# Kernel optimization log

Hardware: AMD Instinct MI355X
Metric: run time of the kernel (lower is better)

The kernel has to match this reference:

```python
import jax, jax.numpy as jnp
import numpy as np

B, S, D, H, HD = 4, 2048, 1024, 16, 64
MLP = 4 * D
ROPE_BASE = 10000.0
TARGET_SPARSITY = 0.2


def _rotate_half(t):
    return jnp.concatenate([-t[..., HD // 2:], t[..., :HD // 2]], axis=-1)


def setup_inputs() -> dict:
    key = jax.random.key(0)
    ks = jax.random.split(key, 10)
    s = 0.02
    return {
        "x": jax.random.normal(ks[0], (B, S, D), jnp.float32),
        "gate_w": jax.random.normal(ks[1], (D, 1), jnp.float32) * s,
        "gate_b": jnp.zeros((1,), jnp.float32),
        "wq": jax.random.normal(ks[2], (D, D), jnp.float32) * s,
        "wk": jax.random.normal(ks[3], (D, D), jnp.float32) * s,
        "wv": jax.random.normal(ks[4], (D, D), jnp.float32) * s,
        "wo": jax.random.normal(ks[5], (D, D), jnp.float32) * s,
        "conv_w": jax.random.normal(ks[6], (D, 3), jnp.float32) * s,  # depthwise k=3
        "conv_b": jnp.zeros((D,), jnp.float32),
        "mlp_w1": jax.random.normal(ks[7], (D, MLP), jnp.float32) * s,
        "mlp_b1": jnp.zeros((MLP,), jnp.float32),
        "mlp_w2": jax.random.normal(ks[8], (MLP, D), jnp.float32) * s,
        "mlp_b2": jnp.zeros((D,), jnp.float32),
    }


def reference(x, gate_w, gate_b, wq, wk, wv, wo, conv_w, conv_b,
              mlp_w1, mlp_b1, mlp_w2, mlp_b2):
    # --- Router (eval path: hard threshold, mask_ste == active mask) ---
    logits = x @ gate_w + gate_b                    # [B,S,1]
    probs = jax.nn.sigmoid(logits)
    aux_loss = (probs.mean() - TARGET_SPARSITY) ** 2
    mask = (probs > 0.5).astype(x.dtype)            # [B,S,1]

    # --- Reflexive stream: causal depthwise conv (left pad 2) + MLP ---
    xp = jnp.pad(x, ((0, 0), (2, 0), (0, 0)))       # [B,S+2,D]
    x_conv = (xp[:, 0:S] * conv_w[:, 0]
              + xp[:, 1:S + 1] * conv_w[:, 1]
              + xp[:, 2:S + 2] * conv_w[:, 2] + conv_b)
    shallow = jax.nn.relu(x_conv @ mlp_w1 + mlp_b1) @ mlp_w2 + mlp_b2

    # --- Contextual stream: RoPE causal attention, queries gated by router ---
    q = (x @ wq).reshape(B, S, H, HD)
    k = (x @ wk).reshape(B, S, H, HD)
    v = (x @ wv).reshape(B, S, H, HD)

    pos = jnp.arange(S)
    inv_freq = 1.0 / (ROPE_BASE ** (jnp.arange(0, HD, 2, dtype=jnp.float32) / HD))
    freqs = pos[:, None].astype(jnp.float32) * inv_freq[None, :]
    emb = jnp.concatenate([freqs, freqs], axis=-1)  # [S,HD]
    cos = jnp.cos(emb)[None, :, None, :]
    sin = jnp.sin(emb)[None, :, None, :]
    q = q * cos + _rotate_half(q) * sin
    k = k * cos + _rotate_half(k) * sin

    scale = 1.0 / np.sqrt(HD)
    scores = jnp.einsum('bqhd,bkhd->bhqk', q, k) * scale
    causal = pos[:, None] >= pos[None, :]           # [S,S]
    scores = jnp.where(causal[None, None], scores, jnp.finfo(scores.dtype).min)
    attn = jax.nn.softmax(scores, axis=-1)
    ctx = jnp.einsum('bhqk,bkhd->bqhd', attn, v).reshape(B, S, D)
    ctx = (ctx @ wo) * mask                         # scatter back: only active queries contribute

    out = x + shallow + ctx
    return out, aux_loss
```

## Files before the change

### kernel.cpp

```cpp
#include <hip/hip_runtime.h>
#include <hip/hip_bf16.h>

#define DDIM 1024
#define SLEN 2048
#define NTOK 8192
#define MLPD 4096

typedef float f32x4 __attribute__((ext_vector_type(4)));
typedef __bf16 bf16x8 __attribute__((ext_vector_type(8)));

__device__ __forceinline__ void async16(void* lds, const void* g) {
  __builtin_amdgcn_global_load_lds(
      (__attribute__((address_space(1))) void*)g,
      (__attribute__((address_space(3))) void*)lds, 16, 0, 0);
}

__global__ __launch_bounds__(256) void prep_kernel(
    const float* __restrict__ x, const float* __restrict__ gate_w,
    const float* __restrict__ gate_b, const float* __restrict__ conv_w,
    const float* __restrict__ conv_b, __bf16* __restrict__ xb,
    __bf16* __restrict__ xcb, float* __restrict__ maskp,
    float* __restrict__ probsp) {
  const int tok = blockIdx.x, t = threadIdx.x;
  const int s = tok & (SLEN - 1);
  const float* xr = x + (size_t)tok * DDIM;
  float4 v = ((const float4*)xr)[t];
  float4 g = ((const float4*)gate_w)[t];
  float part = v.x * g.x + v.y * g.y + v.z * g.z + v.w * g.w;
#pragma unroll
  for (int d = 32; d; d >>= 1) part += __shfl_down(part, d);
  __shared__ float ws4[4];
  const int lane = t & 63, w = t >> 6;
  if (lane == 0) ws4[w] = part;
  __syncthreads();
  if (t == 0) {
    float logit = ws4[0] + ws4[1] + ws4[2] + ws4[3] + gate_b[0];
    float prob = 1.f / (1.f + __expf(-logit));
    probsp[tok] = prob;
    maskp[tok] = prob > 0.5f ? 1.f : 0.f;
  }
  union { ushort4 u; __bf16 b[4]; } xo;
  xo.b[0] = (__bf16)v.x; xo.b[1] = (__bf16)v.y;
  xo.b[2] = (__bf16)v.z; xo.b[3] = (__bf16)v.w;
  ((ushort4*)(xb + (size_t)tok * DDIM))[t] = xo.u;
  float4 zero4 = {0.f, 0.f, 0.f, 0.f};
  float4 m1 = (s >= 1) ? ((const float4*)(xr - DDIM))[t] : zero4;
  float4 m2 = (s >= 2) ? ((const float4*)(xr - 2 * DDIM))[t] : zero4;
  int d0 = t * 4;
  float vv[4] = {v.x, v.y, v.z, v.w};
  float a1[4] = {m1.x, m1.y, m1.z, m1.w};
  float a2[4] = {m2.x, m2.y, m2.z, m2.w};
  union { ushort4 u; __bf16 b[4]; } co;
#pragma unroll
  for (int i = 0; i < 4; ++i) {
    float c0 = conv_w[(d0 + i) * 3 + 0];
    float c1 = conv_w[(d0 + i) * 3 + 1];
    float c2 = conv_w[(d0 + i) * 3 + 2];
    float r = a2[i] * c0 + a1[i] * c1 + vv[i] * c2 + conv_b[d0 + i];
    co.b[i] = (__bf16)r;
  }
  ((ushort4*)(xcb + (size_t)tok * DDIM))[t] = co.u;
}

__global__ __launch_bounds__(256) void tcast_kernel(const float* __restrict__ src,
                                                    __bf16* __restrict__ dst,
                                                    int K, int N) {
  __shared__ __bf16 tile[64][65];
  const int n0 = blockIdx.x * 64, k0 = blockIdx.y * 64;
  const int t = threadIdx.x;
  const int cr = (t & 15) * 4;
#pragma unroll
  for (int i = 0; i < 4; ++i) {
    int rr = (t >> 4) + i * 16;
    float4 v = *(const float4*)(src + (size_t)(k0 + rr) * N + n0 + cr);
    tile[rr][cr + 0] = (__bf16)v.x; tile[rr][cr + 1] = (__bf16)v.y;
    tile[rr][cr + 2] = (__bf16)v.z; tile[rr][cr + 3] = (__bf16)v.w;
  }
  __syncthreads();
#pragma unroll
  for (int i = 0; i < 2; ++i) {
    int c = t + i * 256;
    int nl = c >> 3, koff = (c & 7) * 8;
    union { uint4 u; __bf16 b[8]; } o;
#pragma unroll
    for (int j = 0; j < 8; ++j) o.b[j] = tile[koff + j][nl];
    *(uint4*)(dst + (size_t)(n0 + nl) * K + k0 + koff) = o.u;
  }
}

template <int EPI>
__global__ __launch_bounds__(256, 3) void gemm_bt(
    const __bf16* __restrict__ A, const __bf16* __restrict__ Bt,
    const float* __restrict__ bias, const float* __restrict__ xres,
    const float* __restrict__ maskp, __bf16* __restrict__ Cb,
    float* __restrict__ Cf, int M, int N, int K) {
  __shared__ char smem[32768];
  char* As = smem;
  char* Bs = smem + 16384;
  const int t = threadIdx.x, lane = t & 63, w = t >> 6;
  const int m0 = blockIdx.y * 128, n0 = blockIdx.x * 128;
  const int wm = (w >> 1) * 64, wn = (w & 1) * 64;
  f32x4 acc[4][4] = {};
  const int nk = K >> 6;
  for (int kt = 0; kt < nk; ++kt) {
    const int k0 = kt << 6;
#pragma unroll
    for (int rd = 0; rd < 4; ++rd) {
      int o = ((rd * 4 + w) << 10) + (lane << 4);
      int row = o >> 7;
      int us = ((o >> 4) & 7) ^ (row & 7);
      async16(As + o, A + (size_t)(m0 + row) * K + k0 + us * 8);
      async16(Bs + o, Bt + (size_t)(n0 + row) * K + k0 + us * 8);
    }
    __syncthreads();
#pragma unroll
    for (int ks = 0; ks < 2; ++ks) {
      bf16x8 af[4], bfr[4];
#pragma unroll
      for (int mt = 0; mt < 4; ++mt) {
        int row = wm + mt * 16 + (lane & 15);
        int u = (ks * 4 + (lane >> 4)) ^ (row & 7);
        af[mt] = *(const bf16x8*)(As + row * 128 + u * 16);
      }
#pragma unroll
      for (int nt = 0; nt < 4; ++nt) {
        int row = wn + nt * 16 + (lane & 15);
        int u = (ks * 4 + (lane >> 4)) ^ (row & 7);
        bfr[nt] = *(const bf16x8*)(Bs + row * 128 + u * 16);
      }
#pragma unroll
      for (int mt = 0; mt < 4; ++mt)
#pragma unroll
        for (int nt = 0; nt < 4; ++nt)
          acc[mt][nt] = __builtin_amdgcn_mfma_f32_16x16x32_bf16(
              af[mt], bfr[nt], acc[mt][nt], 0, 0, 0);
    }
    __syncthreads();
  }
#pragma unroll
  for (int mt = 0; mt < 4; ++mt)
#pragma unroll
    for (int nt = 0; nt < 4; ++nt)
#pragma unroll
      for (int r = 0; r < 4; ++r) {
        int row = m0 + wm + mt * 16 + ((lane >> 4) << 2) + r;
        int col = n0 + wn + nt * 16 + (lane & 15);
        float v = acc[mt][nt][r];
        size_t idx = (size_t)row * N + col;
        if constexpr (EPI == 0) {
          Cb[idx] = (__bf16)v;
        } else if constexpr (EPI == 1) {
          v += bias[col];
          Cb[idx] = (__bf16)fmaxf(v, 0.f);
        } else if constexpr (EPI == 2) {
          Cf[idx] = xres[idx] + v + bias[col];
        } else {
          Cf[idx] += maskp[row] * v;
        }
      }
}

__global__ __launch_bounds__(256) void rope_kernel(__bf16* __restrict__ qkv) {
  const int tok = blockIdx.x, t = threadIdx.x;
  const int s = tok & (SLEN - 1);
#pragma unroll
  for (int pp = 0; pp < 2; ++pp) {
    int p = t + pp * 256;
    int h = p >> 5, i = p & 31;
    float invf = __powf(10000.f, -(float)i * (1.f / 32.f));
    float fr = (float)s * invf;
    float sn = sinf(fr), cs = cosf(fr);
    __bf16* qp = qkv + (size_t)tok * 3072 + h * 64 + i;
    float xq = (float)qp[0], yq = (float)qp[32];
    qp[0] = (__bf16)(xq * cs - yq * sn);
    qp[32] = (__bf16)(yq * cs + xq * sn);
    __bf16* kp = qp + 1024;
    float xk = (float)kp[0], yk = (float)kp[32];
    kp[0] = (__bf16)(xk * cs - yk * sn);
    kp[32] = (__bf16)(yk * cs + xk * sn);
  }
}

__device__ __forceinline__ void scatterV(char* Vdst, int w, int lane,
                                         float4 va, float4 vb) {
  union { float4 f; __bf16 bv[8]; } u0, u1;
  u0.f = va; u1.f = vb;
#pragma unroll
  for (int j = 0; j < 8; ++j) {
    int d = w * 8 + j;
    int by = d * 128 + (((lane >> 3) ^ (d & 7)) << 4) + ((lane & 7) << 1);
    *(__bf16*)(Vdst + by) = u0.bv[j];
    int d2 = d + 32;
    int by2 = d2 * 128 + (((lane >> 3) ^ (d2 & 7)) << 4) + ((lane & 7) << 1);
    *(__bf16*)(Vdst + by2) = u1.bv[j];
  }
}

__global__ __launch_bounds__(256, 3) void attn_kernel(const __bf16* __restrict__ qkv,
                                                      __bf16* __restrict__ ctx) {
  __shared__ char sm[49152];
  const int t = threadIdx.x, lane = t & 63, w = t >> 6;
  const int c = lane & 15, g = lane >> 4, g4 = g * 4;
  const int bh = blockIdx.y, h = bh & 15, b = bh >> 4;
  const size_t tokbase = (size_t)b * SLEN;
  const __bf16* qg = qkv + tokbase * 3072 + h * 64;
  const __bf16* kg = qg + 1024;
  const __bf16* vg = qg + 2048;
  const float SCL = 0.125f * 1.44269504f;
  char* Ps = sm + (w << 12);

  for (int ph = 0; ph < 2; ++ph) {
    const int qt = ph == 0 ? (int)blockIdx.x : 15 - (int)blockIdx.x;
    const int q0 = qt * 128;
    int cur = 0;
#pragma unroll
    for (int rd = 0; rd < 4; ++rd) {
      int o = ((rd * 4 + w) << 10) + (lane << 4);
      int row = o >> 7;
      int us = ((o >> 4) & 7) ^ (row & 7);
      async16(sm + o, qg + (size_t)(q0 + row) * 3072 + us * 8);
    }
#pragma unroll
    for (int rd = 0; rd < 2; ++rd) {
      int o = ((rd * 4 + w) << 10) + (lane << 4);
      int row = o >> 7;
      int us = ((o >> 4) & 7) ^ (row & 7);
      async16(sm + 16384 + o, kg + (size_t)row * 3072 + us * 8);
    }
    {
      float4 va = *(const float4*)(vg + (size_t)lane * 3072 + w * 8);
      float4 vb2 = *(const float4*)(vg + (size_t)lane * 3072 + w * 8 + 32);
      scatterV(sm + 32768, w, lane, va, vb2);
    }
    __syncthreads();
    bf16x8 qb[2][2];
#pragma unroll
    for (int mt = 0; mt < 2; ++mt)
#pragma unroll
      for (int ks = 0; ks < 2; ++ks) {
        int row = w * 32 + mt * 16 + c;
        int u = (ks * 4 + g) ^ (row & 7);
        qb[mt][ks] = *(const bf16x8*)(sm + row * 128 + u * 16);
      }

    float m_run[2] = {-1e30f, -1e30f}, l_run[2] = {0.f, 0.f};
    f32x4 o_acc[2][4] = {};
    const int nkt = (q0 + 128) >> 6;
    const int wrow0 = q0 + w * 32;

    for (int kt = 0; kt < nkt; ++kt) {
      const int k0 = kt << 6;
      char* Kc = sm + 16384 + cur * 8192;
      char* Vc = sm + 32768 + cur * 8192;
      const bool pref = (kt + 1) < nkt;
      float4 va, vb2;
      if (pref) {
        const int kn0 = k0 + 64;
        char* Kn = sm + 16384 + (cur ^ 1) * 8192;
#pragma unroll
        for (int rd = 0; rd < 2; ++rd) {
          int o = ((rd * 4 + w) << 10) + (lane << 4);
          int row = o >> 7;
          int us = ((o >> 4) & 7) ^ (row & 7);
          async16(Kn + o, kg + (size_t)(kn0 + row) * 3072 + us * 8);
        }
        va = *(const float4*)(vg + (size_t)(kn0 + lane) * 3072 + w * 8);
        vb2 = *(const float4*)(vg + (size_t)(kn0 + lane) * 3072 + w * 8 + 32);
      }
      if (k0 <= wrow0 + 31) {
        f32x4 st[4][2] = {};
#pragma unroll
        for (int ks = 0; ks < 2; ++ks) {
          bf16x8 ka[4];
#pragma unroll
          for (int nt = 0; nt < 4; ++nt) {
            int row = nt * 16 + c;
            int u = (ks * 4 + g) ^ (row & 7);
            ka[nt] = *(const bf16x8*)(Kc + row * 128 + u * 16);
          }
#pragma unroll
          for (int nt = 0; nt < 4; ++nt)
#pragma unroll
            for (int mt = 0; mt < 2; ++mt)
              st[nt][mt] = __builtin_amdgcn_mfma_f32_16x16x32_bf16(
                  ka[nt], qb[mt][ks], st[nt][mt], 0, 0, 0);
        }
        const bool needmask = (k0 + 63) > wrow0;
#pragma unroll
        for (int mt = 0; mt < 2; ++mt) {
          float mx = -1e30f;
          if (needmask) {
            int qglob = wrow0 + mt * 16 + c;
#pragma unroll
            for (int nt = 0; nt < 4; ++nt)
#pragma unroll
              for (int r = 0; r < 4; ++r) {
                float sv = st[nt][mt][r] * SCL;
                if (k0 + nt * 16 + g4 + r > qglob) sv = -1e30f;
                st[nt][mt][r] = sv;
                mx = fmaxf(mx, sv);
              }
          } else {
#pragma unroll
            for (int nt = 0; nt < 4; ++nt)
#pragma unroll
              for (int r = 0; r < 4; ++r) {
                float sv = st[nt][mt][r] * SCL;
                st[nt][mt][r] = sv;
                mx = fmaxf(mx, sv);
              }
          }
          mx = fmaxf(mx, __shfl_xor(mx, 16));
          mx = fmaxf(mx, __shfl_xor(mx, 32));
          const bool skip = __all(mx - m_run[mt] <= 8.f) != 0;
          float mnew = skip ? m_run[mt] : fmaxf(m_run[mt], mx);
          float rs = 0.f;
#pragma unroll
          for (int nt = 0; nt < 4; ++nt)
#pragma unroll
            for (int r = 0; r < 4; ++r) {
              float p = __builtin_amdgcn_exp2f(st[nt][mt][r] - mnew);
              st[nt][mt][r] = p;
              rs += p;
            }
          rs += __shfl_xor(rs, 16);
          rs += __shfl_xor(rs, 32);
          if (skip) {
            l_run[mt] += rs;
          } else {
            float fac = __builtin_amdgcn_exp2f(m_run[mt] - mnew);
            m_run[mt] = mnew;
            l_run[mt] = l_run[mt] * fac + rs;
#pragma unroll
            for (int r = 0; r < 4; ++r) {
              float fr = __shfl(fac, g * 20 + r);
#pragma unroll
              for (int dt = 0; dt < 4; ++dt) o_acc[mt][dt][r] *= fr;
            }
          }
          int rowq = mt * 16 + c;
          int rbase = rowq * 128 + 8 * (g & 1);
#pragma unroll
          for (int nt = 0; nt < 4; ++nt) {
            int us = (2 * nt + (g >> 1)) ^ (c & 7);
            union { uint2 v; __bf16 bb[4]; } pp;
            pp.bb[0] = (__bf16)st[nt][mt][0]; pp.bb[1] = (__bf16)st[nt][mt][1];
            pp.bb[2] = (__bf16)st[nt][mt][2]; pp.bb[3] = (__bf16)st[nt][mt][3];
            *(uint2*)(Ps + rbase + us * 16) = pp.v;
          }
        }
#pragma unroll
        for (int ks = 0; ks < 2; ++ks) {
          bf16x8 pa[2], vb[4];
#pragma unroll
          for (int mt = 0; mt < 2; ++mt) {
            int row = mt * 16 + c;
            int u = (ks * 4 + g) ^ (row & 7);
            pa[mt] = *(const bf16x8*)(Ps + row * 128 + u * 16);
          }
#pragma unroll
          for (int dt = 0; dt < 4; ++dt) {
            int row = dt * 16 + c;
            int u = (ks * 4 + g) ^ (row & 7);
            vb[dt] = *(const bf16x8*)(Vc + row * 128 + u * 16);
          }
#pragma unroll
          for (int mt = 0; mt < 2; ++mt)
#pragma unroll
            for (int dt = 0; dt < 4; ++dt)
              o_acc[mt][dt] = __builtin_amdgcn_mfma_f32_16x16x32_bf16(
                  pa[mt], vb[dt], o_acc[mt][dt], 0, 0, 0);
        }
      }
      if (pref) scatterV(sm + 32768 + (cur ^ 1) * 8192, w, lane, va, vb2);
      __syncthreads();
      cur ^= 1;
    }
#pragma unroll
    for (int mt = 0; mt < 2; ++mt)
#pragma unroll
      for (int r = 0; r < 4; ++r) {
        float lr = __shfl(l_run[mt], g * 20 + r);
        float inv = 1.f / lr;
        int tokr = q0 + w * 32 + mt * 16 + g4 + r;
#pragma unroll
        for (int dt = 0; dt < 4; ++dt) {
          int d = dt * 16 + c;
          ctx[(tokbase + tokr) * DDIM + h * 64 + d] =
              (__bf16)(o_acc[mt][dt][r] * inv);
        }
      }
    __syncthreads();
  }
}

__global__ __launch_bounds__(256) void aux_kernel(const float* __restrict__ probsp,
                                                  float* __restrict__ outp) {
  const int t = threadIdx.x;
  float sum = 0.f;
  for (int i = t; i < NTOK; i += 256) sum += probsp[i];
#pragma unroll
  for (int d = 32; d; d >>= 1) sum += __shfl_down(sum, d);
  __shared__ float ws4[4];
  if ((t & 63) == 0) ws4[t >> 6] = sum;
  __syncthreads();
  if (t == 0) {
    float m = (ws4[0] + ws4[1] + ws4[2] + ws4[3]) * (1.f / NTOK) - 0.2f;
    outp[0] = m * m;
  }
}

extern "C" void kernel_launch(void* const* d_in, const int* in_sizes, int n_in,
                              void* d_out, int out_size, void* d_ws, size_t ws_size,
                              hipStream_t stream) {
  const float* x      = (const float*)d_in[0];
  const float* gate_w = (const float*)d_in[1];
  const float* gate_b = (const float*)d_in[2];
  const float* wq     = (const float*)d_in[3];
  const float* wk     = (const float*)d_in[4];
  const float* wv     = (const float*)d_in[5];
  const float* wo     = (const float*)d_in[6];
  const float* conv_w = (const float*)d_in[7];
  const float* conv_b = (const float*)d_in[8];
  const float* mlp_w1 = (const float*)d_in[9];
  const float* mlp_b1 = (const float*)d_in[10];
  const float* mlp_w2 = (const float*)d_in[11];
  const float* mlp_b2 = (const float*)d_in[12];
  float* out = (float*)d_out;

  char* ws = (char*)d_ws;
  const size_t MB = 1ull << 20;
  __bf16* xb     = (__bf16*)(ws + 0);
  __bf16* xcb    = (__bf16*)(ws + 16 * MB);
  __bf16* ctx    = (__bf16*)(ws + 16 * MB);
  __bf16* wqkv_t = (__bf16*)(ws + 32 * MB);
  __bf16* wo_t   = (__bf16*)(ws + 38 * MB);
  __bf16* w1_t   = (__bf16*)(ws + 40 * MB);
  __bf16* w2_t   = (__bf16*)(ws + 48 * MB);
  float*  maskp  = (float*)(ws + 56 * MB);
  float*  probsp = (float*)(ws + 56 * MB + 65536);
  __bf16* h1     = (__bf16*)(ws + 57 * MB);
  __bf16* qkv    = (__bf16*)(ws + 57 * MB);

  prep_kernel<<<NTOK, 256, 0, stream>>>(x, gate_w, gate_b, conv_w, conv_b,
                                        xb, xcb, maskp, probsp);
  tcast_kernel<<<dim3(16, 16), 256, 0, stream>>>(wq, wqkv_t, 1024, 1024);
  tcast_kernel<<<dim3(16, 16), 256, 0, stream>>>(wk, wqkv_t + 1024 * 1024, 1024, 1024);
  tcast_kernel<<<dim3(16, 16), 256, 0, stream>>>(wv, wqkv_t + 2048 * 1024, 1024, 1024);
  tcast_kernel<<<dim3(16, 16), 256, 0, stream>>>(wo, wo_t, 1024, 1024);
  tcast_kernel<<<dim3(64, 16), 256, 0, stream>>>(mlp_w1, w1_t, 1024, 4096);
  tcast_kernel<<<dim3(16, 64), 256, 0, stream>>>(mlp_w2, w2_t, 4096, 1024);

  gemm_bt<1><<<dim3(32, 64), 256, 0, stream>>>(xcb, w1_t, mlp_b1, nullptr, nullptr,
                                               h1, nullptr, NTOK, MLPD, DDIM);
  gemm_bt<2><<<dim3(8, 64), 256, 0, stream>>>(h1, w2_t, mlp_b2, x, nullptr,
                                              nullptr, out, NTOK, DDIM, MLPD);
  gemm_bt<0><<<dim3(24, 64), 256, 0, stream>>>(xb, wqkv_t, nullptr, nullptr, nullptr,
                                               qkv, nullptr, NTOK, 3072, DDIM);
  rope_kernel<<<NTOK, 256, 0, stream>>>(qkv);
  attn_kernel<<<dim3(8, 64), 256, 0, stream>>>(qkv, ctx);
  gemm_bt<3><<<dim3(8, 64), 256, 0, stream>>>(ctx, wo_t, nullptr, nullptr, maskp,
                                              nullptr, out, NTOK, DDIM, DDIM);
  aux_kernel<<<1, 256, 0, stream>>>(probsp, out + (size_t)(out_size - 1));
}
```

Before: 416.4 us.

## Single-buffer attention tiles, one q-tile per block, and share RoPE sin/cos

The attention kernel drops the paired causal q-tile loop and the K/V double buffering. Each block now handles one 128-row q-tile, uses 32KB of LDS instead of 48KB, and runs on a grid twice as large, with the launch bound raised to 4 blocks per CU. The goal is more occupancy and simpler scheduling, paid for by losing the overlap of the next K/V tile load with compute and by having load-imbalanced blocks, longest-first. Separately, the RoPE kernel computes the 32 sin/cos values once per token in shared memory instead of once per thread.

```diff
diff --git a/kernel.cpp b/kernel.cpp
--- a/kernel.cpp
+++ b/kernel.cpp
@@ -161,15 +161,21 @@
 }
 
 __global__ __launch_bounds__(256) void rope_kernel(__bf16* __restrict__ qkv) {
+  __shared__ float snv[32], csv[32];
   const int tok = blockIdx.x, t = threadIdx.x;
   const int s = tok & (SLEN - 1);
+  if (t < 32) {
+    float invf = __builtin_amdgcn_exp2f(-(float)t * (13.28771238f / 32.f));
+    float fr = (float)s * invf;
+    snv[t] = sinf(fr);
+    csv[t] = cosf(fr);
+  }
+  __syncthreads();
 #pragma unroll
   for (int pp = 0; pp < 2; ++pp) {
     int p = t + pp * 256;
     int h = p >> 5, i = p & 31;
-    float invf = __powf(10000.f, -(float)i * (1.f / 32.f));
-    float fr = (float)s * invf;
-    float sn = sinf(fr), cs = cosf(fr);
+    float sn = snv[i], cs = csv[i];
     __bf16* qp = qkv + (size_t)tok * 3072 + h * 64 + i;
     float xq = (float)qp[0], yq = (float)qp[32];
     qp[0] = (__bf16)(xq * cs - yq * sn);
@@ -196,9 +202,9 @@
   }
 }
 
-__global__ __launch_bounds__(256, 3) void attn_kernel(const __bf16* __restrict__ qkv,
+__global__ __launch_bounds__(256, 4) void attn_kernel(const __bf16* __restrict__ qkv,
                                                       __bf16* __restrict__ ctx) {
-  __shared__ char sm[49152];
+  __shared__ char sm[32768];
   const int t = threadIdx.x, lane = t & 63, w = t >> 6;
   const int c = lane & 15, g = lane >> 4, g4 = g * 4;
   const int bh = blockIdx.y, h = bh & 15, b = bh >> 4;
@@ -208,190 +214,170 @@
   const __bf16* vg = qg + 2048;
   const float SCL = 0.125f * 1.44269504f;
   char* Ps = sm + (w << 12);
-
-  for (int ph = 0; ph < 2; ++ph) {
-    const int qt = ph == 0 ? (int)blockIdx.x : 15 - (int)blockIdx.x;
-    const int q0 = qt * 128;
-    int cur = 0;
-#pragma unroll
-    for (int rd = 0; rd < 4; ++rd) {
-      int o = ((rd * 4 + w) << 10) + (lane << 4);
-      int row = o >> 7;
-      int us = ((o >> 4) & 7) ^ (row & 7);
-      async16(sm + o, qg + (size_t)(q0 + row) * 3072 + us * 8);
-    }
+  char* Ks = sm + 16384;
+  char* Vs = sm + 24576;
+
+  const int qt = 15 - (int)blockIdx.x;
+  const int q0 = qt * 128;
+#pragma unroll
+  for (int rd = 0; rd < 4; ++rd) {
+    int o = ((rd * 4 + w) << 10) + (lane << 4);
+    int row = o >> 7;
+    int us = ((o >> 4) & 7) ^ (row & 7);
+    async16(sm + o, qg + (size_t)(q0 + row) * 3072 + us * 8);
+  }
+  __syncthreads();
+  bf16x8 qb[2][2];
+#pragma unroll
+  for (int mt = 0; mt < 2; ++mt)
+#pragma unroll
+    for (int ks = 0; ks < 2; ++ks) {
+      int row = w * 32 + mt * 16 + c;
+      int u = (ks * 4 + g) ^ (row & 7);
+      qb[mt][ks] = *(const bf16x8*)(sm + row * 128 + u * 16);
+    }
+
+  float m_run[2] = {-1e30f, -1e30f}, l_run[2] = {0.f, 0.f};
+  f32x4 o_acc[2][4] = {};
+  const int nkt = (q0 + 128) >> 6;
+  const int wrow0 = q0 + w * 32;
+
+  for (int kt = 0; kt < nkt; ++kt) {
+    const int k0 = kt << 6;
 #pragma unroll
     for (int rd = 0; rd < 2; ++rd) {
       int o = ((rd * 4 + w) << 10) + (lane << 4);
       int row = o >> 7;
       int us = ((o >> 4) & 7) ^ (row & 7);
-      async16(sm + 16384 + o, kg + (size_t)row * 3072 + us * 8);
+      async16(Ks + o, kg + (size_t)(k0 + row) * 3072 + us * 8);
     }
     {
-      float4 va = *(const float4*)(vg + (size_t)lane * 3072 + w * 8);
-      float4 vb2 = *(const float4*)(vg + (size_t)lane * 3072 + w * 8 + 32);
-      scatterV(sm + 32768, w, lane, va, vb2);
+      float4 va = *(const float4*)(vg + (size_t)(k0 + lane) * 3072 + w * 8);
+      float4 vb2 = *(const float4*)(vg + (size_t)(k0 + lane) * 3072 + w * 8 + 32);
+      scatterV(Vs, w, lane, va, vb2);
     }
     __syncthreads();
-    bf16x8 qb[2][2];
-#pragma unroll
-    for (int mt = 0; mt < 2; ++mt)
+    if (k0 <= wrow0 + 31) {
+      f32x4 st[4][2] = {};
 #pragma unroll
       for (int ks = 0; ks < 2; ++ks) {
-        int row = w * 32 + mt * 16 + c;
-        int u = (ks * 4 + g) ^ (row & 7);
-        qb[mt][ks] = *(const bf16x8*)(sm + row * 128 + u * 16);
-      }
-
-    float m_run[2] = {-1e30f, -1e30f}, l_run[2] = {0.f, 0.f};
-    f32x4 o_acc[2][4] = {};
-    const int nkt = (q0 + 128) >> 6;
-    const int wrow0 = q0 + w * 32;
-
-    for (int kt = 0; kt < nkt; ++kt) {
-      const int k0 = kt << 6;
-      char* Kc = sm + 16384 + cur * 8192;
-      char* Vc = sm + 32768 + cur * 8192;
-      const bool pref = (kt + 1) < nkt;
-      float4 va, vb2;
-      if (pref) {
-        const int kn0 = k0 + 64;
-        char* Kn = sm + 16384 + (cur ^ 1) * 8192;
-#pragma unroll
-        for (int rd = 0; rd < 2; ++rd) {
-          int o = ((rd * 4 + w) << 10) + (lane << 4);
-          int row = o >> 7;
-          int us = ((o >> 4) & 7) ^ (row & 7);
-          async16(Kn + o, kg + (size_t)(kn0 + row) * 3072 + us * 8);
-        }
-        va = *(const float4*)(vg + (size_t)(kn0 + lane) * 3072 + w * 8);
-        vb2 = *(const float4*)(vg + (size_t)(kn0 + lane) * 3072 + w * 8 + 32);
-      }
-      if (k0 <= wrow0 + 31) {
-        f32x4 st[4][2] = {};
-#pragma unroll
-        for (int ks = 0; ks < 2; ++ks) {
-          bf16x8 ka[4];
-#pragma unroll
-          for (int nt = 0; nt < 4; ++nt) {
-            int row = nt * 16 + c;
-            int u = (ks * 4 + g) ^ (row & 7);
-            ka[nt] = *(const bf16x8*)(Kc + row * 128 + u * 16);
+        bf16x8 ka[4];
+#pragma unroll
+        for (int nt = 0; nt < 4; ++nt) {
+          int row = nt * 16 + c;
+          int u = (ks * 4 + g) ^ (row & 7);
+          ka[nt] = *(const bf16x8*)(Ks + row * 128 + u * 16);
+        }
+#pragma unroll
+        for (int nt = 0; nt < 4; ++nt)
+#pragma unroll
+          for (int mt = 0; mt < 2; ++mt)
+            st[nt][mt] = __builtin_amdgcn_mfma_f32_16x16x32_bf16(
+                ka[nt], qb[mt][ks], st[nt][mt], 0, 0, 0);
+      }
+      const bool needmask = (k0 + 63) > wrow0;
+#pragma unroll
+      for (int mt = 0; mt < 2; ++mt) {
+        float mx = -1e30f;
+        if (needmask) {
+          int qglob = wrow0 + mt * 16 + c;
+#pragma unroll
+          for (int nt = 0; nt < 4; ++nt)
+#pragma unroll
+            for (int r = 0; r < 4; ++r) {
+              float sv = st[nt][mt][r] * SCL;
+              if (k0 + nt * 16 + g4 + r > qglob) sv = -1e30f;
+              st[nt][mt][r] = sv;
+              mx = fmaxf(mx, sv);
+            }
+        } else {
+#pragma unroll
+          for (int nt = 0; nt < 4; ++nt)
+#pragma unroll
+            for (int r = 0; r < 4; ++r) {
+              float sv = st[nt][mt][r] * SCL;
+              st[nt][mt][r] = sv;
+              mx = fmaxf(mx, sv);
+            }
+        }
+        mx = fmaxf(mx, __shfl_xor(mx, 16));
+        mx = fmaxf(mx, __shfl_xor(mx, 32));
+        const bool skip = __all(mx - m_run[mt] <= 8.f) != 0;
+        float mnew = skip ? m_run[mt] : fmaxf(m_run[mt], mx);
+        float rs = 0.f;
+#pragma unroll
+        for (int nt = 0; nt < 4; ++nt)
+#pragma unroll
+          for (int r = 0; r < 4; ++r) {
+            float p = __builtin_amdgcn_exp2f(st[nt][mt][r] - mnew);
+            st[nt][mt][r] = p;
+            rs += p;
           }
-#pragma unroll
-          for (int nt = 0; nt < 4; ++nt)
-#pragma unroll
-            for (int mt = 0; mt < 2; ++mt)
-              st[nt][mt] = __builtin_amdgcn_mfma_f32_16x16x32_bf16(
-                  ka[nt], qb[mt][ks], st[nt][mt], 0, 0, 0);
-        }
-        const bool needmask = (k0 + 63) > wrow0;
+        rs += __shfl_xor(rs, 16);
+        rs += __shfl_xor(rs, 32);
+        if (skip) {
+          l_run[mt] += rs;
+        } else {
+          float fac = __builtin_amdgcn_exp2f(m_run[mt] - mnew);
+          m_run[mt] = mnew;
+          l_run[mt] = l_run[mt] * fac + rs;
+#pragma unroll
+          for (int r = 0; r < 4; ++r) {
+            float fr = __shfl(fac, g * 20 + r);
+#pragma unroll
+            for (int dt = 0; dt < 4; ++dt) o_acc[mt][dt][r] *= fr;
+          }
+        }
+        int rowq = mt * 16 + c;
+        int rbase = rowq * 128 + 8 * (g & 1);
+#pragma unroll
+        for (int nt = 0; nt < 4; ++nt) {
+          int us = (2 * nt + (g >> 1)) ^ (c & 7);
+          union { uint2 v; __bf16 bb[4]; } pp;
+          pp.bb[0] = (__bf16)st[nt][mt][0]; pp.bb[1] = (__bf16)st[nt][mt][1];
+          pp.bb[2] = (__bf16)st[nt][mt][2]; pp.bb[3] = (__bf16)st[nt][mt][3];
+          *(uint2*)(Ps + rbase + us * 16) = pp.v;
+        }
+      }
+#pragma unroll
+      for (int ks = 0; ks < 2; ++ks) {
+        bf16x8 pa[2], vb[4];
 #pragma unroll
         for (int mt = 0; mt < 2; ++mt) {
-          float mx = -1e30f;
-          if (needmask) {
-            int qglob = wrow0 + mt * 16 + c;
-#pragma unroll
-            for (int nt = 0; nt < 4; ++nt)
-#pragma unroll
-              for (int r = 0; r < 4; ++r) {
-                float sv = st[nt][mt][r] * SCL;
-                if (k0 + nt * 16 + g4 + r > qglob) sv = -1e30f;
-                st[nt][mt][r] = sv;
-                mx = fmaxf(mx, sv);
-              }
-          } else {
-#pragma unroll
-            for (int nt = 0; nt < 4; ++nt)
-#pragma unroll
-              for (int r = 0; r < 4; ++r) {
-                float sv = st[nt][mt][r] * SCL;
-                st[nt][mt][r] = sv;
-                mx = fmaxf(mx, sv);
-              }
-          }
-          mx = fmaxf(mx, __shfl_xor(mx, 16));
-          mx = fmaxf(mx, __shfl_xor(mx, 32));
-          const bool skip = __all(mx - m_run[mt] <= 8.f) != 0;
-          float mnew = skip ? m_run[mt] : fmaxf(m_run[mt], mx);
-          float rs = 0.f;
-#pragma unroll
-          for (int nt = 0; nt < 4; ++nt)
-#pragma unroll
-            for (int r = 0; r < 4; ++r) {
-              float p = __builtin_amdgcn_exp2f(st[nt][mt][r] - mnew);
-              st[nt][mt][r] = p;
-              rs += p;
-            }
-          rs += __shfl_xor(rs, 16);
-          rs += __shfl_xor(rs, 32);
-          if (skip) {
-            l_run[mt] += rs;
-          } else {
-            float fac = __builtin_amdgcn_exp2f(m_run[mt] - mnew);
-            m_run[mt] = mnew;
-            l_run[mt] = l_run[mt] * fac + rs;
-#pragma unroll
-            for (int r = 0; r < 4; ++r) {
-              float fr = __shfl(fac, g * 20 + r);
-#pragma unroll
-              for (int dt = 0; dt < 4; ++dt) o_acc[mt][dt][r] *= fr;
-            }
-          }
-          int rowq = mt * 16 + c;
-          int rbase = rowq * 128 + 8 * (g & 1);
-#pragma unroll
-          for (int nt = 0; nt < 4; ++nt) {
-            int us = (2 * nt + (g >> 1)) ^ (c & 7);
-            union { uint2 v; __bf16 bb[4]; } pp;
-            pp.bb[0] = (__bf16)st[nt][mt][0]; pp.bb[1] = (__bf16)st[nt][mt][1];
-            pp.bb[2] = (__bf16)st[nt][mt][2]; pp.bb[3] = (__bf16)st[nt][mt][3];
-            *(uint2*)(Ps + rbase + us * 16) = pp.v;
-          }
-        }
-#pragma unroll
-        for (int ks = 0; ks < 2; ++ks) {
-          bf16x8 pa[2], vb[4];
-#pragma unroll
-          for (int mt = 0; mt < 2; ++mt) {
-            int row = mt * 16 + c;
-            int u = (ks * 4 + g) ^ (row & 7);
-            pa[mt] = *(const bf16x8*)(Ps + row * 128 + u * 16);
-          }
-#pragma unroll
-          for (int dt = 0; dt < 4; ++dt) {
-            int row = dt * 16 + c;
-            int u = (ks * 4 + g) ^ (row & 7);
-            vb[dt] = *(const bf16x8*)(Vc + row * 128 + u * 16);
-          }
-#pragma unroll
-          for (int mt = 0; mt < 2; ++mt)
-#pragma unroll
-            for (int dt = 0; dt < 4; ++dt)
-              o_acc[mt][dt] = __builtin_amdgcn_mfma_f32_16x16x32_bf16(
-                  pa[mt], vb[dt], o_acc[mt][dt], 0, 0, 0);
-        }
-      }
-      if (pref) scatterV(sm + 32768 + (cur ^ 1) * 8192, w, lane, va, vb2);
-      __syncthreads();
-      cur ^= 1;
-    }
-#pragma unroll
-    for (int mt = 0; mt < 2; ++mt)
-#pragma unroll
-      for (int r = 0; r < 4; ++r) {
-        float lr = __shfl(l_run[mt], g * 20 + r);
-        float inv = 1.f / lr;
-        int tokr = q0 + w * 32 + mt * 16 + g4 + r;
+          int row = mt * 16 + c;
+          int u = (ks * 4 + g) ^ (row & 7);
+          pa[mt] = *(const bf16x8*)(Ps + row * 128 + u * 16);
+        }
 #pragma unroll
         for (int dt = 0; dt < 4; ++dt) {
-          int d = dt * 16 + c;
-          ctx[(tokbase + tokr) * DDIM + h * 64 + d] =
-              (__bf16)(o_acc[mt][dt][r] * inv);
-        }
-      }
+          int row = dt * 16 + c;
+          int u = (ks * 4 + g) ^ (row & 7);
+          vb[dt] = *(const bf16x8*)(Vs + row * 128 + u * 16);
+        }
+#pragma unroll
+        for (int mt = 0; mt < 2; ++mt)
+#pragma unroll
+          for (int dt = 0; dt < 4; ++dt)
+            o_acc[mt][dt] = __builtin_amdgcn_mfma_f32_16x16x32_bf16(
+                pa[mt], vb[dt], o_acc[mt][dt], 0, 0, 0);
+      }
+    }
     __syncthreads();
   }
+#pragma unroll
+  for (int mt = 0; mt < 2; ++mt)
+#pragma unroll
+    for (int r = 0; r < 4; ++r) {
+      float lr = __shfl(l_run[mt], g * 20 + r);
+      float inv = 1.f / lr;
+      int tokr = q0 + w * 32 + mt * 16 + g4 + r;
+#pragma unroll
+      for (int dt = 0; dt < 4; ++dt) {
+        int d = dt * 16 + c;
+        ctx[(tokbase + tokr) * DDIM + h * 64 + d] =
+            (__bf16)(o_acc[mt][dt][r] * inv);
+      }
+    }
 }
 
 __global__ __launch_bounds__(256) void aux_kernel(const float* __restrict__ probsp,
@@ -458,7 +444,7 @@
   gemm_bt<0><<<dim3(24, 64), 256, 0, stream>>>(xb, wqkv_t, nullptr, nullptr, nullptr,
                                                qkv, nullptr, NTOK, 3072, DDIM);
   rope_kernel<<<NTOK, 256, 0, stream>>>(qkv);
-  attn_kernel<<<dim3(8, 64), 256, 0, stream>>>(qkv, ctx);
+  attn_kernel<<<dim3(16, 64), 256, 0, stream>>>(qkv, ctx);
   gemm_bt<3><<<dim3(8, 64), 256, 0, stream>>>(ctx, wo_t, nullptr, nullptr, maskp,
                                               nullptr, out, NTOK, DDIM, DDIM);
   aux_kernel<<<1, 256, 0, stream>>>(probsp, out + (size_t)(out_size - 1));
```

After: 536.2 us. 28.7% more time.
